# Performance work log

Measured on AMD Instinct MI355X. Metric: run time of the kernel, lower is better.

The kernel has to match this reference:

```python
import jax, jax.numpy as jnp
import numpy as np

B, L, D = 8, 2048, 512

def setup_inputs() -> dict:
    key = jax.random.key(0)
    k1, k2 = jax.random.split(key)
    x1 = jax.random.normal(k1, (B, L, D), dtype=jnp.float32)
    x2 = jax.random.normal(k2, (B, L, D), dtype=jnp.float32)
    return {"x1": x1, "x2": x2}

def reference(x1, x2):
    # Mutual cross-attention (inference; dropout disabled).
    d = jnp.asarray(x1.shape[-1], dtype=x1.dtype)
    scale = 1.0 / jnp.sqrt(d)
    # shared score matrix: scores_kq = scores_qk^T
    scores_qk = jnp.einsum('bqd,bkd->bqk', x1, x2) * scale  # (B, L1, L2)
    # row softmax over keys -> attend x2
    w_qk = jax.nn.softmax(scores_qk, axis=-1)
    out_A = jnp.einsum('bqk,bkd->bqd', w_qk, x2)
    # transpose-softmax over queries -> attend x1
    w_kq = jax.nn.softmax(jnp.swapaxes(scores_qk, 1, 2), axis=-1)  # (B, L2, L1)
    out_B = jnp.einsum('bkq,bqd->bkd', w_kq, x1)
    return out_A + out_B
```

## Files before the change

kernel.cpp:

```cpp
#include <hip/hip_runtime.h>
#include <hip/hip_bf16.h>

#define LSEQ 2048
#define DIM  512
#define BR   128
#define BC   32
#define NKT  (LSEQ / BC)
#define SCALE 0.044194173824159216f
#define ARR_ELEMS (8u * 2048u * 512u)

typedef __attribute__((ext_vector_type(8))) short short8;
typedef __attribute__((ext_vector_type(4))) float f32x4;
typedef __attribute__((ext_vector_type(4))) unsigned short us4;

static __device__ __forceinline__ unsigned int pk_bf16(float a, float b) {
  union { __hip_bfloat162 h; unsigned int u; } x;
  x.h = __float22bfloat162_rn(make_float2(a, b));
  return x.u;
}

static __device__ __forceinline__ void async16(const unsigned short* g, unsigned short* l) {
  __builtin_amdgcn_global_load_lds(
      (const __attribute__((address_space(1))) void*)g,
      (__attribute__((address_space(3))) void*)l, 16, 0, 0);
}

__global__ __launch_bounds__(256) void mca_prep(
    const float* __restrict__ x1, const float* __restrict__ x2,
    unsigned short* __restrict__ ws) {
  const int bid = blockIdx.x;
  const int lt = bid & 31;
  const int dt = (bid >> 5) & 7;
  const int ba = bid >> 8;
  const int arr = ba & 1, b = ba >> 1;
  const float* src = (arr ? x2 : x1) + (size_t)b * LSEQ * DIM;
  unsigned short* xb = ws + (size_t)arr * ARR_ELEMS + (size_t)b * LSEQ * DIM;
  unsigned short* xT = ws + (size_t)(2 + arr) * ARR_ELEMS + (size_t)b * DIM * LSEQ;
  const int l0 = lt * 64, d0 = dt * 64;

  __shared__ unsigned short tile[64 * 66];
  const int t = threadIdx.x;
  const int dc = (t & 15) * 4;
  #pragma unroll
  for (int p = 0; p < 4; ++p) {
    int l = p * 16 + (t >> 4);
    float4 v = *(const float4*)(src + (size_t)(l0 + l) * DIM + d0 + dc);
    unsigned int w0 = pk_bf16(v.x, v.y), w1 = pk_bf16(v.z, v.w);
    *(uint2*)(xb + (size_t)(l0 + l) * DIM + d0 + dc) = make_uint2(w0, w1);
    *(unsigned int*)&tile[l * 66 + dc]     = w0;
    *(unsigned int*)&tile[l * 66 + dc + 2] = w1;
  }
  __syncthreads();
  const int d = t >> 2, lp = t & 3;
  union { unsigned short u[8]; uint4 q; } o0, o1;
  #pragma unroll
  for (int j = 0; j < 8; ++j) o0.u[j] = tile[(lp * 16 + j) * 66 + d];
  #pragma unroll
  for (int j = 0; j < 8; ++j) o1.u[j] = tile[(lp * 16 + 8 + j) * 66 + d];
  uint4* dst = (uint4*)(xT + (size_t)(d0 + d) * LSEQ + l0 + lp * 16);
  dst[0] = o0.q;
  dst[1] = o1.q;
}

__global__ __launch_bounds__(512, 2) void mca_mfma(
    const unsigned short* __restrict__ ws, float* __restrict__ out) {
  __shared__ __align__(16) unsigned short kS[2][BC * 512];
  __shared__ __align__(16) unsigned short vS[2][512 * BC];

  const int tid = threadIdx.x;
  const int w = tid >> 6, lane = tid & 63, qd = lane >> 4, cl = lane & 15;
  const int g = blockIdx.x & 15, qt = blockIdx.x >> 4;
  const int dir = g & 1, b = g >> 1;

  const unsigned short* xbQ = ws + (size_t)(dir ? ARR_ELEMS : 0) + (size_t)b * LSEQ * DIM;
  const unsigned short* xbK = ws + (size_t)(dir ? 0 : ARR_ELEMS) + (size_t)b * LSEQ * DIM;
  const unsigned short* xTV = ws + (size_t)(dir ? 2 : 3) * ARR_ELEMS + (size_t)b * DIM * LSEQ;

  short8 qa[16];
  {
    const unsigned short* qrow = xbQ + (size_t)(qt * BR + w * 16 + cl) * DIM + qd * 8;
    #pragma unroll
    for (int ch = 0; ch < 16; ++ch)
      qa[ch] = *(const short8*)(qrow + ch * 32);
  }

  f32x4 accO[32];
  #pragma unroll
  for (int nt = 0; nt < 32; ++nt) accO[nt] = (f32x4){0.f, 0.f, 0.f, 0.f};
  float lsum = 0.f;

  auto stage = [&](int kt) {
    const unsigned short* srcK = xbK + (size_t)kt * BC * DIM;
    unsigned short* dstK = kS[kt & 1];
    #pragma unroll
    for (int i = 0; i < 4; ++i) {
      int r = w * 4 + i;
      async16(srcK + r * 512 + (((lane ^ (r & 7)) & 63) << 3), dstK + r * 512);
    }
    unsigned short* dstV = vS[kt & 1];
    #pragma unroll
    for (int i = 0; i < 4; ++i) {
      int row0 = (w * 4 + i) * 16;
      const unsigned short* srcV =
          xTV + (size_t)(row0 + (lane >> 2)) * LSEQ + kt * BC + (lane & 3) * 8;
      async16(srcV, dstV + row0 * 32);
    }
  };

  stage(0);
  for (int kt = 0; kt < NKT; ++kt) {
    __syncthreads();
    if (kt + 1 < NKT) stage(kt + 1);

    const unsigned short* kb = kS[kt & 1];
    f32x4 t0a = (f32x4){0,0,0,0}, t0b = t0a, t1a = t0a, t1b = t0a;
    #pragma unroll
    for (int ch = 0; ch < 8; ++ch) {
      int phys = (((ch * 4 + qd) ^ (cl & 7)) << 3);
      short8 k0 = *(const short8*)(kb + cl * 512 + phys);
      short8 k1 = *(const short8*)(kb + (16 + cl) * 512 + phys);
      t0a = __builtin_amdgcn_mfma_f32_16x16x32_bf16(k0, qa[ch], t0a, 0, 0, 0);
      t1a = __builtin_amdgcn_mfma_f32_16x16x32_bf16(k1, qa[ch], t1a, 0, 0, 0);
    }
    #pragma unroll
    for (int ch = 8; ch < 16; ++ch) {
      int phys = (((ch * 4 + qd) ^ (cl & 7)) << 3);
      short8 k0 = *(const short8*)(kb + cl * 512 + phys);
      short8 k1 = *(const short8*)(kb + (16 + cl) * 512 + phys);
      t0b = __builtin_amdgcn_mfma_f32_16x16x32_bf16(k0, qa[ch], t0b, 0, 0, 0);
      t1b = __builtin_amdgcn_mfma_f32_16x16x32_bf16(k1, qa[ch], t1b, 0, 0, 0);
    }
    f32x4 s0 = t0a + t0b, s1 = t1a + t1b;

    float p0[4], p1[4];
    #pragma unroll
    for (int r = 0; r < 4; ++r) {
      p0[r] = __expf(s0[r] * SCALE);
      p1[r] = __expf(s1[r] * SCALE);
    }
    lsum += p0[0] + p0[1] + p0[2] + p0[3] + p1[0] + p1[1] + p1[2] + p1[3];

    float tv[8];
    {
      const int sA = ((qd & 1) * 2) * 16 + cl;
      #pragma unroll
      for (int r = 0; r < 4; ++r) {
        float a0 = __shfl(p0[r], sA),      b0 = __shfl(p1[r], sA);
        float a1 = __shfl(p0[r], sA + 16), b1 = __shfl(p1[r], sA + 16);
        tv[r]     = (qd < 2) ? a0 : b0;
        tv[4 + r] = (qd < 2) ? a1 : b1;
      }
    }
    union { unsigned int u[4]; short8 s; } pf;
    pf.u[0] = pk_bf16(tv[0], tv[1]);
    pf.u[1] = pk_bf16(tv[2], tv[3]);
    pf.u[2] = pk_bf16(tv[4], tv[5]);
    pf.u[3] = pk_bf16(tv[6], tv[7]);

    const unsigned short* vb0 = vS[kt & 1] + cl * 32 + qd * 8;
    #pragma unroll
    for (int g4 = 0; g4 < 4; ++g4) {
      short8 vb[8];
      #pragma unroll
      for (int j = 0; j < 8; ++j)
        vb[j] = *(const short8*)(vb0 + (g4 * 8 + j) * 16 * 32);
      #pragma unroll
      for (int j = 0; j < 8; ++j)
        accO[g4 * 8 + j] =
            __builtin_amdgcn_mfma_f32_16x16x32_bf16(pf.s, vb[j], accO[g4 * 8 + j], 0, 0, 0);
    }
  }

  float rs = lsum;
  rs += __shfl_xor(rs, 16);
  rs += __shfl_xor(rs, 32);
  float inv[4];
  #pragma unroll
  for (int r = 0; r < 4; ++r)
    inv[r] = 1.0f / __shfl(rs, qd * 4 + r);

  #pragma unroll
  for (int nt = 0; nt < 32; ++nt) {
    float* orow =
        out + ((size_t)(b * LSEQ + qt * BR + w * 16 + qd * 4)) * DIM + nt * 16 + cl;
    #pragma unroll
    for (int r = 0; r < 4; ++r)
      atomicAdd(orow + (size_t)r * DIM, accO[nt][r] * inv[r]);
  }
}

static __device__ __forceinline__ int kv_addr_fb(int row, int col) {
  return row * 520 + ((((col >> 3) ^ ((row >> 3) & 3))) << 3) + (col & 7);
}

__global__ __launch_bounds__(256, 2) void mca_fallback(
    const float* __restrict__ x1, const float* __restrict__ x2,
    float* __restrict__ out) {
  __shared__ __align__(16) unsigned short kvS[BC * 520];
  __shared__ __align__(16) unsigned short pS[64 * 40];
  __shared__ float lS[64];
  const int tid = threadIdx.x;
  const int w = tid >> 6, lane = tid & 63, qd = lane >> 4, cl = lane & 15;
  const int g = blockIdx.x & 15, qt = blockIdx.x >> 4;
  const int dir = g & 1, b = g >> 1;
  const float* qptr = dir ? x2 : x1;
  const float* kvptr = dir ? x1 : x2;
  short8 qa[16];
  {
    const float* qrow = qptr + ((size_t)(b * LSEQ + qt * 64 + w * 16 + cl)) * DIM + qd * 8;
    #pragma unroll
    for (int ch = 0; ch < 16; ++ch) {
      const float4* p = (const float4*)(qrow + ch * 32);
      float4 v0 = p[0]; float4 v1 = p[1];
      union { unsigned int u[4]; short8 s; } pk;
      pk.u[0] = pk_bf16(v0.x, v0.y); pk.u[1] = pk_bf16(v0.z, v0.w);
      pk.u[2] = pk_bf16(v1.x, v1.y); pk.u[3] = pk_bf16(v1.z, v1.w);
      qa[ch] = pk.s;
    }
  }
  f32x4 accO[4][8];
  #pragma unroll
  for (int mt = 0; mt < 4; ++mt)
    #pragma unroll
    for (int nt = 0; nt < 8; ++nt) accO[mt][nt] = (f32x4){0.f,0.f,0.f,0.f};
  float lsum[4] = {0.f,0.f,0.f,0.f};
  const float* kvbase = kvptr + (size_t)b * LSEQ * DIM;
  for (int kt = 0; kt < LSEQ / BC; ++kt) {
    __syncthreads();
    {
      const float* src = kvbase + (size_t)kt * BC * DIM;
      #pragma unroll
      for (int i = 0; i < 16; ++i) {
        int f = i * 1024 + tid * 4;
        int row = f >> 9, col = f & 511;
        float4 v = *(const float4*)(src + f);
        union { unsigned int u[2]; us4 s; } pk;
        pk.u[0] = pk_bf16(v.x, v.y); pk.u[1] = pk_bf16(v.z, v.w);
        *(us4*)&kvS[kv_addr_fb(row, col)] = pk.s;
      }
    }
    __syncthreads();
    f32x4 s0 = (f32x4){0.f,0.f,0.f,0.f}, s1 = (f32x4){0.f,0.f,0.f,0.f};
    #pragma unroll
    for (int ch = 0; ch < 16; ++ch) {
      int colk = ch * 32 + qd * 8;
      short8 k0 = *(const short8*)&kvS[kv_addr_fb(cl, colk)];
      short8 k1 = *(const short8*)&kvS[kv_addr_fb(16 + cl, colk)];
      s0 = __builtin_amdgcn_mfma_f32_16x16x32_bf16(qa[ch], k0, s0, 0, 0, 0);
      s1 = __builtin_amdgcn_mfma_f32_16x16x32_bf16(qa[ch], k1, s1, 0, 0, 0);
    }
    float p0[4], p1[4];
    #pragma unroll
    for (int r = 0; r < 4; ++r) { p0[r] = __expf(s0[r] * SCALE); p1[r] = __expf(s1[r] * SCALE); }
    #pragma unroll
    for (int r = 0; r < 4; ++r) {
      float u = p0[r] + p1[r];
      u += __shfl_xor(u, 1); u += __shfl_xor(u, 2);
      u += __shfl_xor(u, 4); u += __shfl_xor(u, 8);
      lsum[r] += u;
    }
    #pragma unroll
    for (int r = 0; r < 4; ++r) {
      int row = w * 16 + qd * 4 + r;
      unsigned int pkd = pk_bf16(p0[r], p1[r]);
      pS[row * 40 + cl] = (unsigned short)(pkd & 0xffff);
      pS[row * 40 + 16 + cl] = (unsigned short)(pkd >> 16);
    }
    __syncthreads();
    short8 pf[4];
    #pragma unroll
    for (int mt = 0; mt < 4; ++mt)
      pf[mt] = *(const short8*)&pS[(mt * 16 + cl) * 40 + qd * 8];
    #pragma unroll
    for (int nt = 0; nt < 8; ++nt) {
      int col = w * 128 + nt * 16 + cl;
      int base = qd * 8 * 520 + ((((col >> 3) ^ qd)) << 3) + (col & 7);
      union { unsigned short u[8]; short8 s; } vf;
      #pragma unroll
      for (int j = 0; j < 8; ++j) vf.u[j] = kvS[base + j * 520];
      #pragma unroll
      for (int mt = 0; mt < 4; ++mt)
        accO[mt][nt] = __builtin_amdgcn_mfma_f32_16x16x32_bf16(pf[mt], vf.s, accO[mt][nt], 0, 0, 0);
    }
  }
  if (cl == 0) {
    #pragma unroll
    for (int r = 0; r < 4; ++r) lS[w * 16 + qd * 4 + r] = lsum[r];
  }
  __syncthreads();
  #pragma unroll
  for (int mt = 0; mt < 4; ++mt) {
    float inv[4];
    #pragma unroll
    for (int r = 0; r < 4; ++r) inv[r] = 1.0f / lS[mt * 16 + qd * 4 + r];
    #pragma unroll
    for (int nt = 0; nt < 8; ++nt) {
      int col = w * 128 + nt * 16 + cl;
      float* orow = out + ((size_t)(b * LSEQ + qt * 64 + mt * 16 + qd * 4)) * DIM + col;
      #pragma unroll
      for (int r = 0; r < 4; ++r)
        atomicAdd(orow + (size_t)r * DIM, accO[mt][nt][r] * inv[r]);
    }
  }
}

extern "C" void kernel_launch(void* const* d_in, const int* in_sizes, int n_in,
                              void* d_out, int out_size, void* d_ws, size_t ws_size,
                              hipStream_t stream) {
  const float* x1 = (const float*)d_in[0];
  const float* x2 = (const float*)d_in[1];
  float* out = (float*)d_out;
  hipMemsetAsync(out, 0, (size_t)out_size * sizeof(float), stream);
  if (ws_size >= (size_t)ARR_ELEMS * 2 * 4) {
    mca_prep<<<dim3(4096), dim3(256), 0, stream>>>(x1, x2, (unsigned short*)d_ws);
    mca_mfma<<<dim3(256), dim3(512), 0, stream>>>((const unsigned short*)d_ws, out);
  } else {
    mca_fallback<<<dim3(512), dim3(256), 0, stream>>>(x1, x2, out);
  }
}
```

Baseline: 394.0 us.

## Share P tiles through LDS and split PV output columns across waves

The PV stage changes from each wave computing all 512 output columns for its own 16 query rows to each wave computing a 64-column slice for all 128 query rows of the block. The bf16 probability tiles are written to shared memory and read back by every wave. The prep kernel writes V in a new pre-packed per-key-tile layout, so each V fragment is loaded once from LDS with contiguous staging. The aim is to cut V LDS reads per wave and drop the cross-lane shuffles, at the cost of an extra block-wide barrier per key tile and extra LDS traffic for P.

Result: faster. 338.0 us (-14.2%).

```diff
diff --git a/kernel.cpp b/kernel.cpp
--- a/kernel.cpp
+++ b/kernel.cpp
@@ -34,8 +34,8 @@
   const int ba = bid >> 8;
   const int arr = ba & 1, b = ba >> 1;
   const float* src = (arr ? x2 : x1) + (size_t)b * LSEQ * DIM;
-  unsigned short* xb = ws + (size_t)arr * ARR_ELEMS + (size_t)b * LSEQ * DIM;
-  unsigned short* xT = ws + (size_t)(2 + arr) * ARR_ELEMS + (size_t)b * DIM * LSEQ;
+  unsigned short* xb  = ws + (size_t)arr * ARR_ELEMS + (size_t)b * LSEQ * DIM;
+  unsigned short* xTp = ws + (size_t)(2 + arr) * ARR_ELEMS + (size_t)b * LSEQ * DIM;
   const int l0 = lt * 64, d0 = dt * 64;
 
   __shared__ unsigned short tile[64 * 66];
@@ -57,15 +57,18 @@
   for (int j = 0; j < 8; ++j) o0.u[j] = tile[(lp * 16 + j) * 66 + d];
   #pragma unroll
   for (int j = 0; j < 8; ++j) o1.u[j] = tile[(lp * 16 + 8 + j) * 66 + d];
-  uint4* dst = (uint4*)(xT + (size_t)(d0 + d) * LSEQ + l0 + lp * 16);
-  dst[0] = o0.q;
-  dst[1] = o1.q;
+  const int kt = lt * 2 + (lp >> 1);
+  const int p0 = (lp & 1) * 2;
+  *(uint4*)(xTp + ((size_t)kt * 4 + p0)     * 4096 + (size_t)(d0 + d) * 8) = o0.q;
+  *(uint4*)(xTp + ((size_t)kt * 4 + p0 + 1) * 4096 + (size_t)(d0 + d) * 8) = o1.q;
 }
 
 __global__ __launch_bounds__(512, 2) void mca_mfma(
     const unsigned short* __restrict__ ws, float* __restrict__ out) {
   __shared__ __align__(16) unsigned short kS[2][BC * 512];
-  __shared__ __align__(16) unsigned short vS[2][512 * BC];
+  __shared__ __align__(16) unsigned short vS[2][4 * 512 * 8];
+  __shared__ __align__(16) unsigned short pS[BR * 40];
+  __shared__ float lS[BR];
 
   const int tid = threadIdx.x;
   const int w = tid >> 6, lane = tid & 63, qd = lane >> 4, cl = lane & 15;
@@ -74,7 +77,7 @@
 
   const unsigned short* xbQ = ws + (size_t)(dir ? ARR_ELEMS : 0) + (size_t)b * LSEQ * DIM;
   const unsigned short* xbK = ws + (size_t)(dir ? 0 : ARR_ELEMS) + (size_t)b * LSEQ * DIM;
-  const unsigned short* xTV = ws + (size_t)(dir ? 2 : 3) * ARR_ELEMS + (size_t)b * DIM * LSEQ;
+  const unsigned short* xTV = ws + (size_t)(dir ? 2 : 3) * ARR_ELEMS + (size_t)b * LSEQ * DIM;
 
   short8 qa[16];
   {
@@ -84,33 +87,37 @@
       qa[ch] = *(const short8*)(qrow + ch * 32);
   }
 
-  f32x4 accO[32];
-  #pragma unroll
-  for (int nt = 0; nt < 32; ++nt) accO[nt] = (f32x4){0.f, 0.f, 0.f, 0.f};
+  f32x4 accO[8][4];
+  #pragma unroll
+  for (int i = 0; i < 8; ++i)
+    #pragma unroll
+    for (int j = 0; j < 4; ++j)
+      accO[i][j] = (f32x4){0.f, 0.f, 0.f, 0.f};
   float lsum = 0.f;
 
-  auto stage = [&](int kt) {
-    const unsigned short* srcK = xbK + (size_t)kt * BC * DIM;
-    unsigned short* dstK = kS[kt & 1];
+  auto stageK = [&](int kt) {
+    const unsigned short* src = xbK + (size_t)kt * BC * DIM;
+    unsigned short* dst = (unsigned short*)kS[kt & 1];
     #pragma unroll
     for (int i = 0; i < 4; ++i) {
       int r = w * 4 + i;
-      async16(srcK + r * 512 + (((lane ^ (r & 7)) & 63) << 3), dstK + r * 512);
-    }
-    unsigned short* dstV = vS[kt & 1];
+      async16(src + r * 512 + (((lane ^ (r & 7)) & 63) << 3), dst + r * 512);
+    }
+  };
+  auto stageV = [&](int kt) {
+    const unsigned short* src = xTV + (size_t)kt * 16384;
+    unsigned short* dst = (unsigned short*)vS[kt & 1];
     #pragma unroll
     for (int i = 0; i < 4; ++i) {
-      int row0 = (w * 4 + i) * 16;
-      const unsigned short* srcV =
-          xTV + (size_t)(row0 + (lane >> 2)) * LSEQ + kt * BC + (lane & 3) * 8;
-      async16(srcV, dstV + row0 * 32);
+      int c = w * 4 + i;
+      async16(src + c * 512 + lane * 8, dst + c * 512);
     }
   };
 
-  stage(0);
+  stageK(0); stageV(0);
   for (int kt = 0; kt < NKT; ++kt) {
     __syncthreads();
-    if (kt + 1 < NKT) stage(kt + 1);
+    if (kt + 1 < NKT) { stageK(kt + 1); stageV(kt + 1); }
 
     const unsigned short* kb = kS[kt & 1];
     f32x4 t0a = (f32x4){0,0,0,0}, t0b = t0a, t1a = t0a, t1b = t0a;
@@ -140,52 +147,50 @@
     }
     lsum += p0[0] + p0[1] + p0[2] + p0[3] + p1[0] + p1[1] + p1[2] + p1[3];
 
-    float tv[8];
     {
-      const int sA = ((qd & 1) * 2) * 16 + cl;
-      #pragma unroll
-      for (int r = 0; r < 4; ++r) {
-        float a0 = __shfl(p0[r], sA),      b0 = __shfl(p1[r], sA);
-        float a1 = __shfl(p0[r], sA + 16), b1 = __shfl(p1[r], sA + 16);
-        tv[r]     = (qd < 2) ? a0 : b0;
-        tv[4 + r] = (qd < 2) ? a1 : b1;
-      }
-    }
-    union { unsigned int u[4]; short8 s; } pf;
-    pf.u[0] = pk_bf16(tv[0], tv[1]);
-    pf.u[1] = pk_bf16(tv[2], tv[3]);
-    pf.u[2] = pk_bf16(tv[4], tv[5]);
-    pf.u[3] = pk_bf16(tv[6], tv[7]);
-
-    const unsigned short* vb0 = vS[kt & 1] + cl * 32 + qd * 8;
-    #pragma unroll
-    for (int g4 = 0; g4 < 4; ++g4) {
-      short8 vb[8];
-      #pragma unroll
-      for (int j = 0; j < 8; ++j)
-        vb[j] = *(const short8*)(vb0 + (g4 * 8 + j) * 16 * 32);
-      #pragma unroll
-      for (int j = 0; j < 8; ++j)
-        accO[g4 * 8 + j] =
-            __builtin_amdgcn_mfma_f32_16x16x32_bf16(pf.s, vb[j], accO[g4 * 8 + j], 0, 0, 0);
+      unsigned int a0 = pk_bf16(p0[0], p0[1]), a1 = pk_bf16(p0[2], p0[3]);
+      unsigned int b0 = pk_bf16(p1[0], p1[1]), b1 = pk_bf16(p1[2], p1[3]);
+      unsigned short* pr = &pS[(w * 16 + cl) * 40 + qd * 4];
+      *(uint2*)pr        = make_uint2(a0, a1);
+      *(uint2*)(pr + 16) = make_uint2(b0, b1);
+    }
+    __syncthreads();
+
+    const unsigned short* vb0 = vS[kt & 1] + qd * 4096 + (w * 64 + cl) * 8;
+    short8 vb[4];
+    #pragma unroll
+    for (int dt4 = 0; dt4 < 4; ++dt4)
+      vb[dt4] = *(const short8*)(vb0 + dt4 * 16 * 8);
+    #pragma unroll
+    for (int qtile = 0; qtile < 8; ++qtile) {
+      short8 pf = *(const short8*)&pS[(qtile * 16 + cl) * 40 + qd * 8];
+      #pragma unroll
+      for (int dt4 = 0; dt4 < 4; ++dt4)
+        accO[qtile][dt4] =
+            __builtin_amdgcn_mfma_f32_16x16x32_bf16(pf, vb[dt4], accO[qtile][dt4], 0, 0, 0);
     }
   }
 
   float rs = lsum;
   rs += __shfl_xor(rs, 16);
   rs += __shfl_xor(rs, 32);
-  float inv[4];
-  #pragma unroll
-  for (int r = 0; r < 4; ++r)
-    inv[r] = 1.0f / __shfl(rs, qd * 4 + r);
-
-  #pragma unroll
-  for (int nt = 0; nt < 32; ++nt) {
-    float* orow =
-        out + ((size_t)(b * LSEQ + qt * BR + w * 16 + qd * 4)) * DIM + nt * 16 + cl;
-    #pragma unroll
-    for (int r = 0; r < 4; ++r)
-      atomicAdd(orow + (size_t)r * DIM, accO[nt][r] * inv[r]);
+  if (qd == 0) lS[w * 16 + cl] = rs;
+  __syncthreads();
+
+  #pragma unroll
+  for (int qtile = 0; qtile < 8; ++qtile) {
+    float inv[4];
+    #pragma unroll
+    for (int r = 0; r < 4; ++r) inv[r] = 1.0f / lS[qtile * 16 + qd * 4 + r];
+    #pragma unroll
+    for (int dt4 = 0; dt4 < 4; ++dt4) {
+      float* orow = out +
+          ((size_t)(b * LSEQ + qt * BR + qtile * 16 + qd * 4)) * DIM +
+          w * 64 + dt4 * 16 + cl;
+      #pragma unroll
+      for (int r = 0; r < 4; ++r)
+        atomicAdd(orow + (size_t)r * DIM, accO[qtile][dt4][r] * inv[r]);
+    }
   }
 }
 
```
